# Kernel tuning notes

Measured on AMD Instinct MI355X. Metric: run time of the kernel, lower is better.

Reference implementation:

```python
import jax, jax.numpy as jnp
import numpy as np

FEATURES = 4096
BATCH = 2048


def setup_inputs() -> dict:
    key = jax.random.key(0)
    kx, kk = jax.random.split(key)
    x = jax.random.normal(kx, (BATCH, FEATURES), dtype=jnp.float32)
    kernel = jax.random.normal(kk, (FEATURES,), dtype=jnp.float32)
    return {"x": x, "kernel": kernel}


def reference(x, kernel):
    n = kernel.shape[0]
    i = jnp.arange(n)[:, None]   # [n,1]
    j = jnp.arange(n)[None, :]   # [1,n]
    idx = i - j                   # Toeplitz offsets
    # W[i,j] = kernel[i-j] if i>=j else 0  (causal lower-triangular Toeplitz)
    W = jnp.where(idx >= 0, kernel[jnp.clip(idx, 0, n - 1)], 0.0)
    # out[b,i] = sum_{j<=i} x[b,j] * kernel[i-j]  == x @ W.T
    return x @ W.T
```

## Files before the change

kernel.cpp:

```cpp
#include <hip/hip_runtime.h>
#include <hip/hip_bf16.h>


typedef unsigned short u16;
typedef __attribute__((ext_vector_type(8))) short  bf16x8;
typedef __attribute__((ext_vector_type(8))) unsigned short u16x8;
typedef __attribute__((ext_vector_type(4))) float  f32x4;

#define KDIM 4096
#define NDIM 4096
#define MDIM 2048
#define KREV_STRIDE 4608
#define KREV_BYTES  (8 * KREV_STRIDE * 2)
#define BSTRIDE 520
#define XB_BYTES  (MDIM * KDIM * 2)
#define PART_BYTES (2 * 256 * 16384 * 4)

static __device__ inline u16 f2bf(float f) {
  unsigned u = __builtin_bit_cast(unsigned, f);
  unsigned r = u + 0x7FFFu + ((u >> 16) & 1u);
  return (u16)(r >> 16);
}

static __device__ inline void async_copy16(const void* g, void* l) {
  __builtin_amdgcn_global_load_lds((const __attribute__((address_space(1))) void*)g,
                                   (__attribute__((address_space(3))) void*)l,
                                   16, 0, 0);
}

__global__ __launch_bounds__(256) void prep(const float* __restrict__ x,
                                            const float* __restrict__ kern,
                                            u16* __restrict__ xb,
                                            u16* __restrict__ krevs,
                                            int conv_blocks) {
  int kb = (int)blockIdx.x - conv_blocks;
  if (kb >= 0) {
    int u = kb * 256 + threadIdx.x;
    for (int a = 0; a < 8; ++a) {
      int t = u + a - 8;
      u16 v = 0;
      if (t >= 0 && t <= 4095) v = f2bf(kern[4095 - t]);
      krevs[a * KREV_STRIDE + u] = v;
    }
  } else {
    size_t i = ((size_t)blockIdx.x * 256 + threadIdx.x) * 8;
    const f32x4* p = (const f32x4*)(x + i);
    f32x4 v0 = p[0], v1 = p[1];
    u16x8 r;
    r[0] = f2bf(v0[0]); r[1] = f2bf(v0[1]); r[2] = f2bf(v0[2]); r[3] = f2bf(v0[3]);
    r[4] = f2bf(v1[0]); r[5] = f2bf(v1[1]); r[6] = f2bf(v1[2]); r[7] = f2bf(v1[3]);
    *(u16x8*)(xb + i) = r;
  }
}

__global__ __launch_bounds__(256) void reduce_parts(const float* __restrict__ partials,
                                                    float* __restrict__ out) {
  const int rb = (int)blockIdx.x;
  const int tileIdx = rb >> 1;
  const int hh = rb & 1;
  const int ct = 16 + (tileIdx >> 4);
  const int mt = tileIdx & 15;
  const f32x4* p0 = (const f32x4*)(partials + (size_t)tileIdx * 16384);
  const f32x4* p1 = (const f32x4*)(partials + (size_t)(256 + tileIdx) * 16384);
  for (int i = 0; i < 8; ++i) {
    int chunk = hh * 2048 + (int)threadIdx.x + i * 256;
    int row = chunk >> 5;
    int c4  = chunk & 31;
    f32x4 v = p0[chunk];
    f32x4 w = p1[chunk];
    v[0]+=w[0]; v[1]+=w[1]; v[2]+=w[2]; v[3]+=w[3];
    *(f32x4*)(out + (size_t)(mt * 128 + row) * NDIM + ct * 128 + c4 * 4) = v;
  }
}

template <bool CONV>
__global__ __launch_bounds__(512, 4) void toeplitz_gemm(const void* __restrict__ Av,
                                                        const u16* __restrict__ krevs,
                                                        float* __restrict__ out,
                                                        float* __restrict__ partials,
                                                        int split_mode) {
  __shared__ __align__(16) char smem_raw[49408];
  u16*   A_all = (u16*)smem_raw;
  u16*   B_all = (u16*)(smem_raw + 32768);
  f32x4* ep    = (f32x4*)smem_raw;

  const int tid  = threadIdx.x;
  const int w    = tid >> 6;
  const int g    = w >> 2;
  const int wl   = w & 3;
  const int lane = tid & 63;
  const int lane16 = lane & 15;
  const int quad   = lane >> 4;
  const int wm = wl >> 1;
  const int wn = wl & 1;

  int ct, mt, s0, cnt, h = 0, split = 0;
  const int b = (int)blockIdx.x;
  if (split_mode) {
    if (b < 640) {
      int p = b / 80, r = b % 80;
      if (r < 48) {
        if (r < 32) { split = 1; ct = 31 - 2 * p; h = r >> 4; mt = r & 15; }
        else        { split = 0; ct = 15 - p;     mt = r - 32; }
      } else        { split = 1; ct = 30 - 2 * p; int r2 = r - 48; h = r2 >> 4; mt = r2 & 15; }
    } else {
      int j = b - 640; split = 0; ct = 7 - (j >> 4); mt = j & 15;
    }
  } else {
    const int rank = (b < 256) ? b : 511 - (b & 255);
    ct = 31 - (rank >> 4); mt = rank & 15;
  }
  if (split) { s0 = h * (ct + 1); cnt = ct + 1; }
  else       { s0 = 0;            cnt = 2 * ct + 2; }

  const int n0 = ct * 128;
  const int m0 = mt * 128;
  const int W  = 3968 - n0;

  int boff[4];
  for (int fn = 0; fn < 4; ++fn) {
    int n_g = n0 + wn * 64 + fn * 16 + lane16;
    int s0f = 4095 - n_g + quad * 8;
    int a   = s0f & 7;
    boff[fn] = a * BSTRIDE + (s0f - a + 8 - W);
  }

  f32x4 acc[4][4] = {};
  const int srow8 = lane >> 3;
  const int ssrc  = ((lane & 7) ^ srow8) * 8;

  const u16*  xb = (const u16*)Av;
  const float* xf = (const float*)Av;
  u16* A_g = A_all + g * 8192;

  auto stageA = [&](int ls) {
    const int k0 = (s0 + ls) * 64;
    if constexpr (CONV) {
      int j    = tid & 255;
      int row  = j >> 1;
      int lh   = j & 1;
      for (int lc = 0; lc < 4; ++lc) {
        int l = lh * 4 + lc;
        int p = l ^ (row & 7);
        const f32x4* px = (const f32x4*)(xf + (size_t)(m0 + row) * KDIM + k0 + l * 8);
        f32x4 v0 = px[0], v1 = px[1];
        u16x8 r;
        r[0]=f2bf(v0[0]); r[1]=f2bf(v0[1]); r[2]=f2bf(v0[2]); r[3]=f2bf(v0[3]);
        r[4]=f2bf(v1[0]); r[5]=f2bf(v1[1]); r[6]=f2bf(v1[2]); r[7]=f2bf(v1[3]);
        *(u16x8*)(&A_g[row * 64 + p * 8]) = r;
      }
    } else {
      for (int c = 0; c < 4; ++c) {
        int g8  = c * 4 + wl;
        int row = g8 * 8 + srow8;
        async_copy16(xb + (size_t)(m0 + row) * KDIM + k0 + ssrc,
                     &A_g[g8 * 512]);
      }
    }
  };
  auto stageB = [&](int c) {
    async_copy16(krevs + w * KREV_STRIDE + W + s0 * 64 + c * 256 + (lane << 3),
                 &B_all[(c & 1) * 4160 + w * BSTRIDE]);
  };

  const int T   = (cnt + 1) >> 1;
  const int nch = (T + 1) >> 1;

  stageB(0);
  stageA(g);

  for (int t = 0;; ++t) {
    __syncthreads();
    if (2 * t + g < cnt) {
      const u16* Bb  = B_all + ((t >> 1) & 1) * 4160;
      const int  ksl = (t & 1) * 128 + g * 64;
      for (int kk = 0; kk < 2; ++kk) {
        bf16x8 af[4];
        const int p = (kk * 4 + quad) ^ (lane16 & 7);
        for (int fm = 0; fm < 4; ++fm) {
          int row = wm * 64 + fm * 16 + lane16;
          af[fm] = *(const bf16x8*)(&A_g[row * 64 + p * 8]);
        }
        bf16x8 bf[4];
        for (int fn = 0; fn < 4; ++fn)
          bf[fn] = *(const bf16x8*)(&Bb[boff[fn] + ksl + kk * 32]);
        for (int fm = 0; fm < 4; ++fm)
          for (int fn = 0; fn < 4; ++fn)
            acc[fm][fn] = __builtin_amdgcn_mfma_f32_16x16x32_bf16(af[fm], bf[fn], acc[fm][fn], 0, 0, 0);
      }
    }
    if (t + 1 == T) break;
    __syncthreads();
    if (2 * (t + 1) + g < cnt) stageA(2 * (t + 1) + g);
    if (!(t & 1) && (t >> 1) + 1 < nch) stageB((t >> 1) + 1);
  }

  const int j = tid & 255;
  for (int r = 0; r < 2; ++r) {
    __syncthreads();
    if (g == 1) {
      for (int fm2 = 0; fm2 < 2; ++fm2)
        for (int fn = 0; fn < 4; ++fn)
          ep[j * 9 + fm2 * 4 + fn] = acc[r * 2 + fm2][fn];
    }
    __syncthreads();
    if (g == 0) {
      for (int fm2 = 0; fm2 < 2; ++fm2)
        for (int fn = 0; fn < 4; ++fn)
          acc[r * 2 + fm2][fn] += ep[j * 9 + fm2 * 4 + fn];
    }
  }

  if (g == 0) {
    if (split) {
      float* pp = partials + (size_t)(h * 256 + (ct - 16) * 16 + mt) * 16384;
      for (int fm = 0; fm < 4; ++fm) {
        int rl = wm * 64 + fm * 16 + quad * 4;
        for (int fn = 0; fn < 4; ++fn) {
          int cl = wn * 64 + fn * 16 + lane16;
          for (int r = 0; r < 4; ++r)
            pp[(rl + r) * 128 + cl] = acc[fm][fn][r];
        }
      }
    } else {
      for (int fm = 0; fm < 4; ++fm) {
        int row_base = m0 + wm * 64 + fm * 16 + quad * 4;
        for (int fn = 0; fn < 4; ++fn) {
          int col = n0 + wn * 64 + fn * 16 + lane16;
          for (int r = 0; r < 4; ++r)
            out[(size_t)(row_base + r) * NDIM + col] = acc[fm][fn][r];
        }
      }
    }
  }
}

extern "C" void kernel_launch(void* const* d_in, const int* in_sizes, int n_in,
                              void* d_out, int out_size, void* d_ws, size_t ws_size,
                              hipStream_t stream) {
  const float* x    = (const float*)d_in[0];
  const float* kern = (const float*)d_in[1];
  float* out = (float*)d_out;

  u16*   krevs    = (u16*)d_ws;
  u16*   xb       = (u16*)((char*)d_ws + KREV_BYTES);
  float* partials = (float*)((char*)d_ws + KREV_BYTES + XB_BYTES);

  const size_t need_fast  = (size_t)KREV_BYTES + XB_BYTES;
  const size_t need_split = need_fast + PART_BYTES;

  if (ws_size >= need_split) {
    prep<<<4096 + 18, 256, 0, stream>>>(x, kern, xb, krevs, 4096);
    toeplitz_gemm<false><<<768, 512, 0, stream>>>(xb, krevs, out, partials, 1);
    reduce_parts<<<512, 256, 0, stream>>>(partials, out);
  } else if (ws_size >= need_fast) {
    prep<<<4096 + 18, 256, 0, stream>>>(x, kern, xb, krevs, 4096);
    toeplitz_gemm<false><<<512, 512, 0, stream>>>(xb, krevs, out, partials, 0);
  } else {
    prep<<<18, 256, 0, stream>>>(x, kern, xb, krevs, 0);
    toeplitz_gemm<true><<<512, 512, 0, stream>>>(x, krevs, out, partials, 0);
  }
}
```

Measured before the change: 127.9 us.

## Pre-transpose bf16 activations into MFMA fragment layout and load A directly from global

The prep kernel now writes x in a k-block-major layout (8-element k chunks contiguous per row), transposing through an LDS tile. The GEMM then loads A fragments straight from global memory into registers, with no LDS staging. This removes the A shared-memory buffer and about half of the barriers, and shrinks LDS use. The cost is that A loads now go through L2/global with no explicit prefetch, so latency is exposed unless occupancy hides it.

Result: slower. 134.5 us (+5.1%).

```diff
diff --git a/kernel.cpp b/kernel.cpp
--- a/kernel.cpp
+++ b/kernel.cpp
@@ -15,6 +15,7 @@
 #define BSTRIDE 520
 #define XB_BYTES  (MDIM * KDIM * 2)
 #define PART_BYTES (2 * 256 * 16384 * 4)
+#define KBSTRIDE (MDIM * 8)
 
 static __device__ inline u16 f2bf(float f) {
   unsigned u = __builtin_bit_cast(unsigned, f);
@@ -22,6 +23,13 @@
   return (u16)(r >> 16);
 }
 
+static __device__ inline u16x8 cvt8(f32x4 v0, f32x4 v1) {
+  u16x8 r;
+  r[0]=f2bf(v0[0]); r[1]=f2bf(v0[1]); r[2]=f2bf(v0[2]); r[3]=f2bf(v0[3]);
+  r[4]=f2bf(v1[0]); r[5]=f2bf(v1[1]); r[6]=f2bf(v1[2]); r[7]=f2bf(v1[3]);
+  return r;
+}
+
 static __device__ inline void async_copy16(const void* g, void* l) {
   __builtin_amdgcn_global_load_lds((const __attribute__((address_space(1))) void*)g,
                                    (__attribute__((address_space(3))) void*)l,
@@ -30,9 +38,10 @@
 
 __global__ __launch_bounds__(256) void prep(const float* __restrict__ x,
                                             const float* __restrict__ kern,
-                                            u16* __restrict__ xb,
+                                            u16* __restrict__ xbT,
                                             u16* __restrict__ krevs,
                                             int conv_blocks) {
+  __shared__ u16 tile[64][72];
   int kb = (int)blockIdx.x - conv_blocks;
   if (kb >= 0) {
     int u = kb * 256 + threadIdx.x;
@@ -43,13 +52,28 @@
       krevs[a * KREV_STRIDE + u] = v;
     }
   } else {
-    size_t i = ((size_t)blockIdx.x * 256 + threadIdx.x) * 8;
-    const f32x4* p = (const f32x4*)(x + i);
-    f32x4 v0 = p[0], v1 = p[1];
-    u16x8 r;
-    r[0] = f2bf(v0[0]); r[1] = f2bf(v0[1]); r[2] = f2bf(v0[2]); r[3] = f2bf(v0[3]);
-    r[4] = f2bf(v1[0]); r[5] = f2bf(v1[1]); r[6] = f2bf(v1[2]); r[7] = f2bf(v1[3]);
-    *(u16x8*)(xb + i) = r;
+    const int m0 = ((int)blockIdx.x & 31) * 64;
+    const int k0 = ((int)blockIdx.x >> 5) * 64;
+    const int t  = threadIdx.x;
+    {
+      int r  = t >> 2;
+      int kc = (t & 3) * 16;
+      const f32x4* px = (const f32x4*)(x + (size_t)(m0 + r) * KDIM + k0 + kc);
+      f32x4 v0 = px[0], v1 = px[1], v2 = px[2], v3 = px[3];
+      u16x8 a = cvt8(v0, v1), b = cvt8(v2, v3);
+      *(u16x8*)&tile[r][kc]     = a;
+      *(u16x8*)&tile[r][kc + 8] = b;
+    }
+    __syncthreads();
+    {
+      int kbb = t >> 5;
+      int mm  = t & 31;
+      for (int hh = 0; hh < 2; ++hh) {
+        int m = mm + hh * 32;
+        u16x8 v = *(const u16x8*)&tile[m][kbb * 8];
+        *(u16x8*)(xbT + (size_t)(k0 / 8 + kbb) * KBSTRIDE + (size_t)(m0 + m) * 8) = v;
+      }
+    }
   }
 }
 
@@ -79,10 +103,9 @@
                                                         float* __restrict__ out,
                                                         float* __restrict__ partials,
                                                         int split_mode) {
-  __shared__ __align__(16) char smem_raw[49408];
-  u16*   A_all = (u16*)smem_raw;
-  u16*   B_all = (u16*)(smem_raw + 32768);
-  f32x4* ep    = (f32x4*)smem_raw;
+  __shared__ __align__(16) char smem[36864];
+  u16*   B_all = (u16*)smem;
+  f32x4* ep    = (f32x4*)smem;
 
   const int tid  = threadIdx.x;
   const int w    = tid >> 6;
@@ -126,38 +149,11 @@
   }
 
   f32x4 acc[4][4] = {};
-  const int srow8 = lane >> 3;
-  const int ssrc  = ((lane & 7) ^ srow8) * 8;
-
-  const u16*  xb = (const u16*)Av;
-  const float* xf = (const float*)Av;
-  u16* A_g = A_all + g * 8192;
-
-  auto stageA = [&](int ls) {
-    const int k0 = (s0 + ls) * 64;
-    if constexpr (CONV) {
-      int j    = tid & 255;
-      int row  = j >> 1;
-      int lh   = j & 1;
-      for (int lc = 0; lc < 4; ++lc) {
-        int l = lh * 4 + lc;
-        int p = l ^ (row & 7);
-        const f32x4* px = (const f32x4*)(xf + (size_t)(m0 + row) * KDIM + k0 + l * 8);
-        f32x4 v0 = px[0], v1 = px[1];
-        u16x8 r;
-        r[0]=f2bf(v0[0]); r[1]=f2bf(v0[1]); r[2]=f2bf(v0[2]); r[3]=f2bf(v0[3]);
-        r[4]=f2bf(v1[0]); r[5]=f2bf(v1[1]); r[6]=f2bf(v1[2]); r[7]=f2bf(v1[3]);
-        *(u16x8*)(&A_g[row * 64 + p * 8]) = r;
-      }
-    } else {
-      for (int c = 0; c < 4; ++c) {
-        int g8  = c * 4 + wl;
-        int row = g8 * 8 + srow8;
-        async_copy16(xb + (size_t)(m0 + row) * KDIM + k0 + ssrc,
-                     &A_g[g8 * 512]);
-      }
-    }
-  };
+
+  const u16*   xbT = (const u16*)Av;
+  const float* xf  = (const float*)Av;
+  const u16* abase = xbT + (size_t)(m0 + wm * 64 + lane16) * 8 + (size_t)quad * KBSTRIDE;
+
   auto stageB = [&](int c) {
     async_copy16(krevs + w * KREV_STRIDE + W + s0 * 64 + c * 256 + (lane << 3),
                  &B_all[(c & 1) * 4160 + w * BSTRIDE]);
@@ -167,19 +163,30 @@
   const int nch = (T + 1) >> 1;
 
   stageB(0);
-  stageA(g);
-
-  for (int t = 0;; ++t) {
-    __syncthreads();
+
+  for (int t = 0; t < T; ++t) {
+    if (!(t & 1)) {
+      __syncthreads();
+      int c1 = (t >> 1) + 1;
+      if (c1 < nch) stageB(c1);
+    }
     if (2 * t + g < cnt) {
       const u16* Bb  = B_all + ((t >> 1) & 1) * 4160;
       const int  ksl = (t & 1) * 128 + g * 64;
+      const int  sg  = s0 + 2 * t + g;
       for (int kk = 0; kk < 2; ++kk) {
         bf16x8 af[4];
-        const int p = (kk * 4 + quad) ^ (lane16 & 7);
-        for (int fm = 0; fm < 4; ++fm) {
-          int row = wm * 64 + fm * 16 + lane16;
-          af[fm] = *(const bf16x8*)(&A_g[row * 64 + p * 8]);
+        if constexpr (CONV) {
+          for (int fm = 0; fm < 4; ++fm) {
+            const float* px = xf + (size_t)(m0 + wm * 64 + fm * 16 + lane16) * KDIM
+                                 + sg * 64 + kk * 32 + quad * 8;
+            u16x8 r = cvt8(*(const f32x4*)px, *(const f32x4*)(px + 4));
+            af[fm] = *(bf16x8*)&r;
+          }
+        } else {
+          const u16* ap = abase + (size_t)(sg * 8 + kk * 4) * KBSTRIDE;
+          for (int fm = 0; fm < 4; ++fm)
+            af[fm] = *(const bf16x8*)(ap + fm * 128);
         }
         bf16x8 bf[4];
         for (int fn = 0; fn < 4; ++fn)
@@ -189,10 +196,6 @@
             acc[fm][fn] = __builtin_amdgcn_mfma_f32_16x16x32_bf16(af[fm], bf[fn], acc[fm][fn], 0, 0, 0);
       }
     }
-    if (t + 1 == T) break;
-    __syncthreads();
-    if (2 * (t + 1) + g < cnt) stageA(2 * (t + 1) + g);
-    if (!(t & 1) && (t >> 1) + 1 < nch) stageB((t >> 1) + 1);
   }
 
   const int j = tid & 255;
@@ -243,21 +246,21 @@
   float* out = (float*)d_out;
 
   u16*   krevs    = (u16*)d_ws;
-  u16*   xb       = (u16*)((char*)d_ws + KREV_BYTES);
+  u16*   xbT      = (u16*)((char*)d_ws + KREV_BYTES);
   float* partials = (float*)((char*)d_ws + KREV_BYTES + XB_BYTES);
 
   const size_t need_fast  = (size_t)KREV_BYTES + XB_BYTES;
   const size_t need_split = need_fast + PART_BYTES;
 
   if (ws_size >= need_split) {
-    prep<<<4096 + 18, 256, 0, stream>>>(x, kern, xb, krevs, 4096);
-    toeplitz_gemm<false><<<768, 512, 0, stream>>>(xb, krevs, out, partials, 1);
+    prep<<<2048 + 18, 256, 0, stream>>>(x, kern, xbT, krevs, 2048);
+    toeplitz_gemm<false><<<768, 512, 0, stream>>>(xbT, krevs, out, partials, 1);
     reduce_parts<<<512, 256, 0, stream>>>(partials, out);
   } else if (ws_size >= need_fast) {
-    prep<<<4096 + 18, 256, 0, stream>>>(x, kern, xb, krevs, 4096);
-    toeplitz_gemm<false><<<512, 512, 0, stream>>>(xb, krevs, out, partials, 0);
+    prep<<<2048 + 18, 256, 0, stream>>>(x, kern, xbT, krevs, 2048);
+    toeplitz_gemm<false><<<512, 512, 0, stream>>>(xbT, krevs, out, partials, 0);
   } else {
-    prep<<<18, 256, 0, stream>>>(x, kern, xb, krevs, 0);
+    prep<<<18, 256, 0, stream>>>(x, kern, xbT, krevs, 0);
     toeplitz_gemm<true><<<512, 512, 0, stream>>>(x, krevs, out, partials, 0);
   }
 }
```
